# Optimization experiments

Measured on AMD Instinct MI355X. Metric: run time of the kernel, lower is better.

Reference implementation:

```python
import math
import jax, jax.numpy as jnp
import numpy as np

TOPK = 13
NUM_CLASSES = 80
ALPHA = 1.0
BETA = 6.0
EPS = 1e-9


def _ciou(b1, b2, eps=1e-7):
    """CIoU between broadcastable xyxy boxes b1 (gt) and b2 (pred); matches bbox_iou(xywh=False, CIoU=True)."""
    b1x1, b1y1, b1x2, b1y2 = (b1[..., 0], b1[..., 1], b1[..., 2], b1[..., 3])
    b2x1, b2y1, b2x2, b2y2 = (b2[..., 0], b2[..., 1], b2[..., 2], b2[..., 3])
    w1, h1 = b1x2 - b1x1, b1y2 - b1y1 + eps
    w2, h2 = b2x2 - b2x1, b2y2 - b2y1 + eps
    inter = (jnp.clip(jnp.minimum(b1x2, b2x2) - jnp.maximum(b1x1, b2x1), 0.0, None)
             * jnp.clip(jnp.minimum(b1y2, b2y2) - jnp.maximum(b1y1, b2y1), 0.0, None))
    union = w1 * h1 + w2 * h2 - inter + eps
    iou = inter / union
    cw = jnp.maximum(b1x2, b2x2) - jnp.minimum(b1x1, b2x1)
    ch = jnp.maximum(b1y2, b2y2) - jnp.minimum(b1y1, b2y1)
    c2 = cw * cw + ch * ch + eps
    rho2 = ((b2x1 + b2x2 - b1x1 - b1x2) ** 2 + (b2y1 + b2y2 - b1y1 - b1y2) ** 2) / 4.0
    v = (4.0 / math.pi ** 2) * (jnp.arctan(w2 / h2) - jnp.arctan(w1 / h1)) ** 2
    alpha = jax.lax.stop_gradient(v / (v - iou + (1.0 + eps)))  # torch.no_grad() block
    return iou - (rho2 / c2 + v * alpha)


def setup_inputs() -> dict:
    key = jax.random.key(0)
    ks = jax.random.split(key, 7)
    bs, M, nc, img = 16, 128, NUM_CLASSES, 640
    # YOLO anchor points for 640x640, strides 8/16/32 -> 8400 points (pixel coords)
    pts = []
    for s in (8, 16, 32):
        n = img // s
        g = (jnp.arange(n, dtype=jnp.float32) + 0.5) * s
        yv, xv = jnp.meshgrid(g, g, indexing='ij')
        pts.append(jnp.stack([xv, yv], -1).reshape(-1, 2))
    anc_points = jnp.concatenate(pts, 0)  # (8400, 2)
    na = anc_points.shape[0]
    pd_scores = jax.random.uniform(ks[0], (bs, na, nc), dtype=jnp.float32)
    # predicted boxes: xyxy around each anchor point
    cxy = anc_points[None] + jax.random.normal(ks[1], (bs, na, 2)) * 4.0
    wh = jax.random.uniform(ks[2], (bs, na, 2), minval=4.0, maxval=96.0)
    pd_bboxes = jnp.concatenate([cxy - wh / 2, cxy + wh / 2], -1)
    # gt boxes: xyxy in image coords
    g_cxy = jax.random.uniform(ks[3], (bs, M, 2), minval=0.0, maxval=640.0)
    g_wh = jax.random.uniform(ks[4], (bs, M, 2), minval=16.0, maxval=200.0)
    gt_bboxes = jnp.concatenate([g_cxy - g_wh / 2, g_cxy + g_wh / 2], -1)
    gt_labels = jax.random.randint(ks[5], (bs, M, 1), 0, nc, dtype=jnp.int32)
    mask_gt = (jax.random.uniform(ks[6], (bs, M, 1)) < 0.8).astype(jnp.float32)
    return {'pd_scores': pd_scores, 'pd_bboxes': pd_bboxes, 'anc_points': anc_points,
            'gt_labels': gt_labels, 'gt_bboxes': gt_bboxes, 'mask_gt': mask_gt}


def reference(pd_scores, pd_bboxes, anc_points, gt_labels, gt_bboxes, mask_gt):
    bs, na, nc = pd_scores.shape
    M = gt_bboxes.shape[1]
    dt = pd_scores.dtype

    # ---- select_candidates_in_gts: anchor center strictly inside gt box ----
    lt = gt_bboxes[:, :, None, :2]   # (bs,M,1,2)
    rb = gt_bboxes[:, :, None, 2:]   # (bs,M,1,2)
    anc = anc_points[None, None]     # (1,1,na,2)
    d_min = jnp.minimum((anc - lt).min(-1), (rb - anc).min(-1))  # (bs,M,na)
    mask_in_gts = (d_min > EPS).astype(dt)

    # ---- get_box_metrics (dense, masked where torch left zeros) ----
    mask = (mask_in_gts * mask_gt) > 0  # (bs,M,na) bool
    lbl = gt_labels[..., 0]             # (bs,M) int
    # pd_scores[b, :, label] -> (bs,M,na)
    gathered = pd_scores[jnp.arange(bs)[:, None], :, lbl]
    bbox_scores = jnp.where(mask, gathered, 0.0)
    ciou = _ciou(gt_bboxes[:, :, None, :], pd_bboxes[:, None, :, :])  # (bs,M,na)
    overlaps = jnp.where(mask, jnp.clip(ciou, 0.0, None), 0.0)
    align_metric = bbox_scores ** ALPHA * overlaps ** BETA

    # ---- select_topk_candidates ----
    _, topk_idxs = jax.lax.top_k(align_metric, TOPK)            # (bs,M,TOPK)
    topk_idxs = jnp.where(mask_gt > 0, topk_idxs, 0)            # masked_fill_(~topk_mask, 0)
    row_off = (jnp.arange(bs * M, dtype=topk_idxs.dtype) * na).reshape(bs, M, 1)
    counts = (jnp.zeros(bs * M * na, jnp.int32)
              .at[(topk_idxs + row_off).ravel()].add(1)
              .reshape(bs, M, na))
    mask_topk = jnp.where(counts > 1, 0, counts).astype(dt)     # drop anchors hit >1 time per gt

    mask_pos = mask_topk * mask_in_gts * mask_gt                # (bs,M,na)

    # ---- select_highest_overlaps: resolve anchors claimed by multiple gts ----
    fg_mask = mask_pos.sum(1)                                   # (bs,na)
    mask_multi = fg_mask[:, None, :] > 1                        # (bs,1,na)
    max_ov_idx = overlaps.argmax(1)                             # (bs,na)
    is_max = jax.nn.one_hot(max_ov_idx, M, dtype=dt).transpose(0, 2, 1)  # (bs,M,na)
    mask_pos = jnp.where(mask_multi, is_max, mask_pos)
    fg_mask = mask_pos.sum(1)
    target_gt_idx = mask_pos.argmax(1)                          # (bs,na)

    # ---- get_targets ----
    flat_idx = target_gt_idx + jnp.arange(bs, dtype=target_gt_idx.dtype)[:, None] * M
    target_labels = jnp.clip(gt_labels.reshape(-1)[flat_idx], 0, None)     # (bs,na)
    target_bboxes = gt_bboxes.reshape(-1, 4)[flat_idx]                     # (bs,na,4)
    target_scores = jax.nn.one_hot(target_labels, nc, dtype=dt)
    target_scores = jnp.where(fg_mask[..., None] > 0, target_scores, 0.0)

    # ---- normalization of target scores ----
    am = align_metric * mask_pos
    pos_am = am.max(-1, keepdims=True)                          # (bs,M,1)
    pos_ov = (overlaps * mask_pos).max(-1, keepdims=True)       # (bs,M,1)
    norm = (am * pos_ov / (pos_am + EPS)).max(1)[..., None]     # (bs,na,1)
    target_scores = target_scores * norm

    return (target_labels, target_bboxes, target_scores, fg_mask > 0, target_gt_idx)
```

## Files before the change

### kernel.cpp

```cpp
#include <hip/hip_runtime.h>
#include <math.h>

constexpr int BS = 16;
constexpr int NA = 8400;
constexpr int NC = 80;
constexpr int MG = 128;
constexpr int TK = 13;
constexpr int NCAND = 1536;
constexpr int QCAP = 65536;

constexpr int OFF_LBL = 0;
constexpr int OFF_BB  = OFF_LBL + BS * NA;
constexpr int OFF_SC  = OFF_BB  + BS * NA * 4;
constexpr int OFF_FG  = OFF_SC  + BS * NA * NC;
constexpr int OFF_TG  = OFF_FG  + BS * NA;

__device__ __forceinline__ float ciou_pre(float gx, float gy, float gz, float gw,
                                          float px, float py, float pz, float pw,
                                          float dat) {
    const float eps = 1e-7f;
    float w1 = gz - gx, h1 = gw - gy + eps;
    float w2 = pz - px, h2 = pw - py + eps;
    float iw = fmaxf(fminf(gz, pz) - fmaxf(gx, px), 0.f);
    float ih = fmaxf(fminf(gw, pw) - fmaxf(gy, py), 0.f);
    float inter = iw * ih;
    float uni = w1 * h1 + w2 * h2 - inter + eps;
    float iou = inter / uni;
    float cw = fmaxf(gz, pz) - fminf(gx, px);
    float ch = fmaxf(gw, pw) - fminf(gy, py);
    float c2 = cw * cw + ch * ch + eps;
    float dx = px + pz - gx - gz;
    float dy = py + pw - gy - gw;
    float rho2 = (dx * dx + dy * dy) * 0.25f;
    float v = 0.4052847345693511f * dat * dat;
    float alpha = v / (v - iou + (1.f + eps));
    return iou - (rho2 / c2 + v * alpha);
}

__device__ __forceinline__ float ciou_f(float gx, float gy, float gz, float gw,
                                        float px, float py, float pz, float pw) {
    const float eps = 1e-7f;
    float dat = atanf((pz - px) / (pw - py + eps)) - atanf((gz - gx) / (gw - gy + eps));
    return ciou_pre(gx, gy, gz, gw, px, py, pz, pw, dat);
}

__device__ __forceinline__ bool inside_gt(float ax, float ay,
                                          float gx, float gy, float gz, float gw) {
    float d = fminf(fminf(ax - gx, ay - gy), fminf(gz - ax, gw - ay));
    return d > 1e-9f;
}

__device__ __forceinline__ void anchor_xy(int a, float& ax, float& ay) {
    if (a < 6400)      { int iy = a / 80;        int ix = a - iy * 80 - 0;    ax = (ix + 0.5f) * 8.f;  ay = (iy + 0.5f) * 8.f; }
    else if (a < 8000) { int r = a - 6400; int iy = r / 40; int ix = r - iy * 40; ax = (ix + 0.5f) * 16.f; ay = (iy + 0.5f) * 16.f; }
    else               { int r = a - 8000; int iy = r / 20; int ix = r - iy * 20; ax = (ix + 0.5f) * 32.f; ay = (iy + 0.5f) * 32.f; }
}

__global__ __launch_bounds__(64) void k_topk(
    const float* __restrict__ pd_scores, const float* __restrict__ pd_bboxes,
    const int* __restrict__ gt_labels, const float* __restrict__ gt_bboxes,
    const float* __restrict__ mask_gt,
    int* __restrict__ fg_cnt, int* __restrict__ fg_m)
{
    __shared__ float cv[NCAND];
    __shared__ int   ca[NCAND];
    __shared__ int   s_cnt;
    __shared__ unsigned s_pm;

    int bm = blockIdx.x;
    if (mask_gt[bm] <= 0.f) return;
    int b = bm >> 7;
    int m = bm & (MG - 1);
    int tid = threadIdx.x;

    if (tid == 0) { s_cnt = 0; s_pm = 0u; }
    __syncthreads();

    const float4 g = *reinterpret_cast<const float4*>(gt_bboxes + bm * 4);
    const int lbl = gt_labels[bm];
    const float* pbb = pd_bboxes + (size_t)b * NA * 4;
    const float* psc = pd_scores + (size_t)b * NA * NC;
    const float at_g = atanf((g.z - g.x) / (g.w - g.y + 1e-7f));

    auto do_level = [&](float s, int n, int base) {
        int xlo = max(0, (int)floorf(g.x / s - 0.5f) - 1);
        int xhi = min(n - 1, (int)ceilf(g.z / s - 0.5f) + 1);
        int ylo = max(0, (int)floorf(g.y / s - 0.5f) - 1);
        int yhi = min(n - 1, (int)ceilf(g.w / s - 0.5f) + 1);
        int w = xhi - xlo + 1, h = yhi - ylo + 1;
        if (w <= 0 || h <= 0) return;
        int cnt = w * h;
        for (int idx = tid; idx < cnt; idx += 64) {
            int iy = ylo + idx / w;
            int ix = xlo + idx - (idx / w) * w;
            float ax = (ix + 0.5f) * s;
            float ay = (iy + 0.5f) * s;
            if (!inside_gt(ax, ay, g.x, g.y, g.z, g.w)) continue;
            int a = base + iy * n + ix;
            float4 p = *reinterpret_cast<const float4*>(pbb + (size_t)a * 4);
            float dat = atanf((p.z - p.x) / (p.w - p.y + 1e-7f)) - at_g;
            float ov = fmaxf(ciou_pre(g.x, g.y, g.z, g.w, p.x, p.y, p.z, p.w, dat), 0.f);
            float sc = psc[(size_t)a * NC + lbl];
            float ov2 = ov * ov;
            float al = sc * ov2 * ov2 * ov2;
            if (al > 0.f) {
                int slot = atomicAdd(&s_cnt, 1);
                if (slot < NCAND) { cv[slot] = al; ca[slot] = a; }
                if (a < 32) atomicOr(&s_pm, 1u << a);
            }
        }
    };
    do_level(8.f, 80, 0);
    do_level(16.f, 40, 6400);
    do_level(32.f, 20, 8000);
    __syncthreads();

    int npos = min(s_cnt, NCAND);
    int rounds = min(npos, TK);
    int* fgc = fg_cnt + b * NA;
    int* fgm = fg_m + b * NA;

    for (int k = 0; k < rounds; ++k) {
        float bv = -1.f; int bk = 0x7fffffff;
        for (int p = tid; p < npos; p += 64) {
            float v = cv[p];
            int key = (ca[p] << 11) | p;
            if (v > bv || (v == bv && key < bk)) { bv = v; bk = key; }
        }
        #pragma unroll
        for (int off = 32; off > 0; off >>= 1) {
            float v2 = __shfl_down(bv, off);
            int   k2 = __shfl_down(bk, off);
            if (v2 > bv || (v2 == bv && k2 < bk)) { bv = v2; bk = k2; }
        }
        if (tid == 0) {
            int slot = bk & 2047;
            int a = bk >> 11;
            cv[slot] = -1.f;
            atomicAdd(&fgc[a], 1);
            fgm[a] = m;
        }
        __syncthreads();
    }

    if (tid == 0) {
        int need = TK - rounds;
        unsigned pm = s_pm;
        for (int idx = 0; idx < 32 && need > 0; ++idx) {
            if (!((pm >> idx) & 1u)) {
                float ax = (idx + 0.5f) * 8.f, ay = 4.f;
                if (inside_gt(ax, ay, g.x, g.y, g.z, g.w)) {
                    atomicAdd(&fgc[idx], 1);
                    fgm[idx] = m;
                }
                --need;
            }
        }
    }
}

__global__ __launch_bounds__(256) void k_assign(
    const float* __restrict__ pd_scores, const float* __restrict__ pd_bboxes,
    const int* __restrict__ gt_labels, const float* __restrict__ gt_bboxes,
    const float* __restrict__ mask_gt,
    const int* __restrict__ fg_cnt, const int* __restrict__ fg_m,
    float* __restrict__ out, float* __restrict__ am_ws,
    int* __restrict__ gi_ws, int* __restrict__ lbl_ws,
    unsigned* __restrict__ pos_am, unsigned* __restrict__ pos_ov,
    int* __restrict__ multi_cnt, int* __restrict__ multi_q)
{
    __shared__ int s_cnt, s_base;
    int tid = threadIdx.x;
    if (tid == 0) s_cnt = 0;
    __syncthreads();

    int i = blockIdx.x * 256 + tid;
    int cnt = fg_cnt[i];
    bool multi = cnt > 1;

    unsigned long long mk = __ballot(multi);
    int lane = tid & 63;
    int rank = __popcll(mk & ((1ull << lane) - 1ull));
    int wsum = __popcll(mk);
    int wbase = 0;
    if (lane == 0 && wsum) wbase = atomicAdd(&s_cnt, wsum);
    wbase = __shfl(wbase, 0);
    __syncthreads();
    if (tid == 0 && s_cnt) s_base = atomicAdd(multi_cnt, s_cnt);
    __syncthreads();

    if (multi) {
        multi_q[s_base + wbase + rank] = i;
        return;
    }

    int b = i / NA, a = i - b * NA;
    int t = (cnt == 1) ? fg_m[i] : 0;
    int gi = b * MG + t;
    float4 g = *reinterpret_cast<const float4*>(gt_bboxes + gi * 4);
    int lraw = gt_labels[gi];
    int lbl = max(lraw, 0);

    if (cnt == 1) {
        float am = 0.f, ovv = 0.f;
        if (mask_gt[gi] > 0.f) {
            float ax, ay; anchor_xy(a, ax, ay);
            if (inside_gt(ax, ay, g.x, g.y, g.z, g.w)) {
                float4 p = *reinterpret_cast<const float4*>(pd_bboxes + (size_t)i * 4);
                float ov = fmaxf(ciou_f(g.x, g.y, g.z, g.w, p.x, p.y, p.z, p.w), 0.f);
                float sc = pd_scores[(size_t)i * NC + lraw];
                float ov2 = ov * ov;
                am = sc * ov2 * ov2 * ov2;
                ovv = ov;
            }
        }
        atomicMax(&pos_am[gi], __float_as_uint(am));
        atomicMax(&pos_ov[gi], __float_as_uint(ovv));
        am_ws[i] = am; gi_ws[i] = gi; lbl_ws[i] = lbl;
    } else {
        gi_ws[i] = -1;
    }

    out[OFF_LBL + i] = (float)lbl;
    reinterpret_cast<float4*>(out + OFF_BB)[i] = g;
    out[OFF_FG + i] = cnt ? 1.f : 0.f;
    out[OFF_TG + i] = (float)t;
}

__global__ __launch_bounds__(256) void k_fix(
    const float* __restrict__ pd_scores, const float* __restrict__ pd_bboxes,
    const int* __restrict__ gt_labels, const float* __restrict__ gt_bboxes,
    const float* __restrict__ mask_gt,
    const int* __restrict__ multi_cnt, const int* __restrict__ multi_q,
    float* __restrict__ out, float* __restrict__ am_ws,
    int* __restrict__ gi_ws, int* __restrict__ lbl_ws,
    unsigned* __restrict__ pos_am, unsigned* __restrict__ pos_ov)
{
    int gtid = blockIdx.x * 256 + threadIdx.x;
    int wave = gtid >> 6;
    int lane = gtid & 63;
    int nwaves = (gridDim.x * 256) >> 6;
    int qn = *multi_cnt;

    for (int qi = wave; qi < qn; qi += nwaves) {
        int i = multi_q[qi];
        int b = i / NA, a = i - b * NA;
        float ax, ay; anchor_xy(a, ax, ay);
        float4 p = *reinterpret_cast<const float4*>(pd_bboxes + (size_t)i * 4);
        float at_p = atanf((p.z - p.x) / (p.w - p.y + 1e-7f));

        auto ovm = [&](int mm) -> float {
            int gi = b * MG + mm;
            float ov = 0.f;
            if (mask_gt[gi] > 0.f) {
                float4 gg = *reinterpret_cast<const float4*>(gt_bboxes + gi * 4);
                if (inside_gt(ax, ay, gg.x, gg.y, gg.z, gg.w)) {
                    float dat = at_p - atanf((gg.z - gg.x) / (gg.w - gg.y + 1e-7f));
                    ov = fmaxf(ciou_pre(gg.x, gg.y, gg.z, gg.w, p.x, p.y, p.z, p.w, dat), 0.f);
                }
            }
            return ov;
        };
        float ov0 = ovm(lane);
        float ov1 = ovm(lane + 64);
        float bov; int bm_;
        if (ov1 > ov0) { bov = ov1; bm_ = lane + 64; }
        else           { bov = ov0; bm_ = lane; }
        #pragma unroll
        for (int off = 32; off > 0; off >>= 1) {
            float v2 = __shfl_down(bov, off);
            int   m2 = __shfl_down(bm_, off);
            if (v2 > bov || (v2 == bov && m2 < bm_)) { bov = v2; bm_ = m2; }
        }
        if (lane == 0) {
            int t = bm_;
            int gi = b * MG + t;
            int lraw = gt_labels[gi];
            int lbl = max(lraw, 0);
            float am = 0.f;
            if (bov > 0.f) {
                float sc = pd_scores[(size_t)i * NC + lraw];
                float o2 = bov * bov;
                am = sc * o2 * o2 * o2;
            }
            atomicMax(&pos_am[gi], __float_as_uint(am));
            atomicMax(&pos_ov[gi], __float_as_uint(bov));
            float4 g = *reinterpret_cast<const float4*>(gt_bboxes + gi * 4);
            out[OFF_LBL + i] = (float)lbl;
            reinterpret_cast<float4*>(out + OFF_BB)[i] = g;
            out[OFF_FG + i] = 1.f;
            out[OFF_TG + i] = (float)t;
            am_ws[i] = am; gi_ws[i] = gi; lbl_ws[i] = lbl;
        }
    }
}

__global__ __launch_bounds__(256) void k_scatter(
    const float* __restrict__ am_ws, const int* __restrict__ gi_ws,
    const int* __restrict__ lbl_ws,
    const unsigned* __restrict__ pos_am, const unsigned* __restrict__ pos_ov,
    float* __restrict__ out_scores)
{
    int i = blockIdx.x * 256 + threadIdx.x;
    if (i >= BS * NA) return;
    int gi = gi_ws[i];
    if (gi >= 0) {
        float norm = am_ws[i] * __uint_as_float(pos_ov[gi]) /
                     (__uint_as_float(pos_am[gi]) + 1e-9f);
        out_scores[(size_t)i * NC + lbl_ws[i]] = norm;
    }
}

extern "C" void kernel_launch(void* const* d_in, const int* in_sizes, int n_in,
                              void* d_out, int out_size, void* d_ws, size_t ws_size,
                              hipStream_t stream) {
    const float* pd_scores = (const float*)d_in[0];
    const float* pd_bboxes = (const float*)d_in[1];
    const int*   gt_labels = (const int*)d_in[3];
    const float* gt_bboxes = (const float*)d_in[4];
    const float* mask_gt   = (const float*)d_in[5];
    float* out = (float*)d_out;

    unsigned char* w = (unsigned char*)d_ws;
    size_t off = 0;
    int*      fg_cnt    = (int*)(w + off);      off += (size_t)BS * NA * 4;
    unsigned* pos_am    = (unsigned*)(w + off); off += (size_t)BS * MG * 4;
    unsigned* pos_ov    = (unsigned*)(w + off); off += (size_t)BS * MG * 4;
    int*      multi_cnt = (int*)(w + off);      off += 4;
    size_t zero_bytes = off;
    int*      fg_m      = (int*)(w + off);      off += (size_t)BS * NA * 4;
    float*    am_ws     = (float*)(w + off);    off += (size_t)BS * NA * 4;
    int*      gi_ws     = (int*)(w + off);      off += (size_t)BS * NA * 4;
    int*      lbl_ws    = (int*)(w + off);      off += (size_t)BS * NA * 4;
    int*      multi_q   = (int*)(w + off);      off += (size_t)QCAP * 4;

    hipMemsetAsync(w, 0, zero_bytes, stream);
    hipMemsetAsync(out + OFF_SC, 0, (size_t)BS * NA * NC * sizeof(float), stream);

    k_topk<<<BS * MG, 64, 0, stream>>>(pd_scores, pd_bboxes, gt_labels,
                                       gt_bboxes, mask_gt, fg_cnt, fg_m);

    int nA = BS * NA;
    k_assign<<<nA / 256, 256, 0, stream>>>(
        pd_scores, pd_bboxes, gt_labels, gt_bboxes, mask_gt,
        fg_cnt, fg_m, out, am_ws, gi_ws, lbl_ws, pos_am, pos_ov,
        multi_cnt, multi_q);

    k_fix<<<2048, 256, 0, stream>>>(
        pd_scores, pd_bboxes, gt_labels, gt_bboxes, mask_gt,
        multi_cnt, multi_q, out, am_ws, gi_ws, lbl_ws, pos_am, pos_ov);

    k_scatter<<<nA / 256, 256, 0, stream>>>(am_ws, gi_ws, lbl_ws,
                                            pos_am, pos_ov, out + OFF_SC);
}
```

Measured before the change: 152.8 us.

## Fold multi-assignment fix into assign kernel and write dense scores without memset

Removes the separate k_fix kernel and its work queue: anchors claimed by several GTs now loop over all 128 GTs inside k_assign, reusing GT arctan values cached per GT by k_topk. The large memset of the score tensor plus the sparse scatter is replaced by one kernel that writes every score row as float4, zero or normalized. k_topk moves to 128-thread blocks with a two-wave reduction. This cuts launches and one full pass over the score buffer. The cost is that multi-assigned anchors are resolved serially per thread inside divergent wavefronts.

```diff
diff --git a/kernel.cpp b/kernel.cpp
--- a/kernel.cpp
+++ b/kernel.cpp
@@ -7,7 +7,6 @@
 constexpr int MG = 128;
 constexpr int TK = 13;
 constexpr int NCAND = 1536;
-constexpr int QCAP = 65536;
 
 constexpr int OFF_LBL = 0;
 constexpr int OFF_BB  = OFF_LBL + BS * NA;
@@ -37,13 +36,6 @@
     return iou - (rho2 / c2 + v * alpha);
 }
 
-__device__ __forceinline__ float ciou_f(float gx, float gy, float gz, float gw,
-                                        float px, float py, float pz, float pw) {
-    const float eps = 1e-7f;
-    float dat = atanf((pz - px) / (pw - py + eps)) - atanf((gz - gx) / (gw - gy + eps));
-    return ciou_pre(gx, gy, gz, gw, px, py, pz, pw, dat);
-}
-
 __device__ __forceinline__ bool inside_gt(float ax, float ay,
                                           float gx, float gy, float gz, float gw) {
     float d = fminf(fminf(ax - gx, ay - gy), fminf(gz - ax, gw - ay));
@@ -51,21 +43,24 @@
 }
 
 __device__ __forceinline__ void anchor_xy(int a, float& ax, float& ay) {
-    if (a < 6400)      { int iy = a / 80;        int ix = a - iy * 80 - 0;    ax = (ix + 0.5f) * 8.f;  ay = (iy + 0.5f) * 8.f; }
+    if (a < 6400)      { int iy = a / 80;        int ix = a - iy * 80;           ax = (ix + 0.5f) * 8.f;  ay = (iy + 0.5f) * 8.f; }
     else if (a < 8000) { int r = a - 6400; int iy = r / 40; int ix = r - iy * 40; ax = (ix + 0.5f) * 16.f; ay = (iy + 0.5f) * 16.f; }
     else               { int r = a - 8000; int iy = r / 20; int ix = r - iy * 20; ax = (ix + 0.5f) * 32.f; ay = (iy + 0.5f) * 32.f; }
 }
 
-__global__ __launch_bounds__(64) void k_topk(
+__global__ __launch_bounds__(128) void k_topk(
     const float* __restrict__ pd_scores, const float* __restrict__ pd_bboxes,
     const int* __restrict__ gt_labels, const float* __restrict__ gt_bboxes,
     const float* __restrict__ mask_gt,
-    int* __restrict__ fg_cnt, int* __restrict__ fg_m)
+    int* __restrict__ fg_cnt, int* __restrict__ fg_m,
+    float* __restrict__ at_g_tbl)
 {
     __shared__ float cv[NCAND];
     __shared__ int   ca[NCAND];
     __shared__ int   s_cnt;
     __shared__ unsigned s_pm;
+    __shared__ float s_wv[2];
+    __shared__ int   s_wk[2];
 
     int bm = blockIdx.x;
     if (mask_gt[bm] <= 0.f) return;
@@ -81,6 +76,7 @@
     const float* pbb = pd_bboxes + (size_t)b * NA * 4;
     const float* psc = pd_scores + (size_t)b * NA * NC;
     const float at_g = atanf((g.z - g.x) / (g.w - g.y + 1e-7f));
+    if (tid == 0) at_g_tbl[bm] = at_g;
 
     auto do_level = [&](float s, int n, int base) {
         int xlo = max(0, (int)floorf(g.x / s - 0.5f) - 1);
@@ -90,7 +86,7 @@
         int w = xhi - xlo + 1, h = yhi - ylo + 1;
         if (w <= 0 || h <= 0) return;
         int cnt = w * h;
-        for (int idx = tid; idx < cnt; idx += 64) {
+        for (int idx = tid; idx < cnt; idx += 128) {
             int iy = ylo + idx / w;
             int ix = xlo + idx - (idx / w) * w;
             float ax = (ix + 0.5f) * s;
@@ -122,7 +118,7 @@
 
     for (int k = 0; k < rounds; ++k) {
         float bv = -1.f; int bk = 0x7fffffff;
-        for (int p = tid; p < npos; p += 64) {
+        for (int p = tid; p < npos; p += 128) {
             float v = cv[p];
             int key = (ca[p] << 11) | p;
             if (v > bv || (v == bv && key < bk)) { bv = v; bk = key; }
@@ -133,7 +129,11 @@
             int   k2 = __shfl_down(bk, off);
             if (v2 > bv || (v2 == bv && k2 < bk)) { bv = v2; bk = k2; }
         }
+        int wid = tid >> 6;
+        if ((tid & 63) == 0) { s_wv[wid] = bv; s_wk[wid] = bk; }
+        __syncthreads();
         if (tid == 0) {
+            if (s_wv[1] > bv || (s_wv[1] == bv && s_wk[1] < bk)) { bv = s_wv[1]; bk = s_wk[1]; }
             int slot = bk & 2047;
             int a = bk >> 11;
             cv[slot] = -1.f;
@@ -162,58 +162,69 @@
 __global__ __launch_bounds__(256) void k_assign(
     const float* __restrict__ pd_scores, const float* __restrict__ pd_bboxes,
     const int* __restrict__ gt_labels, const float* __restrict__ gt_bboxes,
-    const float* __restrict__ mask_gt,
+    const float* __restrict__ mask_gt, const float* __restrict__ at_g_tbl,
     const int* __restrict__ fg_cnt, const int* __restrict__ fg_m,
     float* __restrict__ out, float* __restrict__ am_ws,
     int* __restrict__ gi_ws, int* __restrict__ lbl_ws,
-    unsigned* __restrict__ pos_am, unsigned* __restrict__ pos_ov,
-    int* __restrict__ multi_cnt, int* __restrict__ multi_q)
+    unsigned* __restrict__ pos_am, unsigned* __restrict__ pos_ov)
 {
-    __shared__ int s_cnt, s_base;
-    int tid = threadIdx.x;
-    if (tid == 0) s_cnt = 0;
-    __syncthreads();
-
-    int i = blockIdx.x * 256 + tid;
+    int i = blockIdx.x * 256 + threadIdx.x;
     int cnt = fg_cnt[i];
+    int b = i / NA, a = i - b * NA;
+    int gbase = b * MG;
+
+    int t = 0;
+    float bov = -1.f;
     bool multi = cnt > 1;
-
-    unsigned long long mk = __ballot(multi);
-    int lane = tid & 63;
-    int rank = __popcll(mk & ((1ull << lane) - 1ull));
-    int wsum = __popcll(mk);
-    int wbase = 0;
-    if (lane == 0 && wsum) wbase = atomicAdd(&s_cnt, wsum);
-    wbase = __shfl(wbase, 0);
-    __syncthreads();
-    if (tid == 0 && s_cnt) s_base = atomicAdd(multi_cnt, s_cnt);
-    __syncthreads();
-
     if (multi) {
-        multi_q[s_base + wbase + rank] = i;
-        return;
-    }
-
-    int b = i / NA, a = i - b * NA;
-    int t = (cnt == 1) ? fg_m[i] : 0;
-    int gi = b * MG + t;
+        float ax, ay; anchor_xy(a, ax, ay);
+        float4 p = *reinterpret_cast<const float4*>(pd_bboxes + (size_t)i * 4);
+        float at_p = atanf((p.z - p.x) / (p.w - p.y + 1e-7f));
+        for (int mm = 0; mm < MG; ++mm) {
+            int gi = gbase + mm;
+            float ov = 0.f;
+            if (mask_gt[gi] > 0.f) {
+                float4 gg = *reinterpret_cast<const float4*>(gt_bboxes + gi * 4);
+                if (inside_gt(ax, ay, gg.x, gg.y, gg.z, gg.w)) {
+                    float dat = at_p - at_g_tbl[gi];
+                    ov = fmaxf(ciou_pre(gg.x, gg.y, gg.z, gg.w, p.x, p.y, p.z, p.w, dat), 0.f);
+                }
+            }
+            if (ov > bov) { bov = ov; t = mm; }
+        }
+    } else if (cnt == 1) {
+        t = fg_m[i];
+    }
+
+    int gi = gbase + t;
     float4 g = *reinterpret_cast<const float4*>(gt_bboxes + gi * 4);
     int lraw = gt_labels[gi];
     int lbl = max(lraw, 0);
 
-    if (cnt == 1) {
-        float am = 0.f, ovv = 0.f;
+    float am = 0.f, ovv = 0.f;
+    if (multi) {
+        if (bov > 0.f) {
+            float sc = pd_scores[(size_t)i * NC + lraw];
+            float o2 = bov * bov;
+            am = sc * o2 * o2 * o2;
+            ovv = bov;
+        }
+    } else if (cnt == 1) {
         if (mask_gt[gi] > 0.f) {
             float ax, ay; anchor_xy(a, ax, ay);
             if (inside_gt(ax, ay, g.x, g.y, g.z, g.w)) {
                 float4 p = *reinterpret_cast<const float4*>(pd_bboxes + (size_t)i * 4);
-                float ov = fmaxf(ciou_f(g.x, g.y, g.z, g.w, p.x, p.y, p.z, p.w), 0.f);
+                float dat = atanf((p.z - p.x) / (p.w - p.y + 1e-7f)) - at_g_tbl[gi];
+                float ov = fmaxf(ciou_pre(g.x, g.y, g.z, g.w, p.x, p.y, p.z, p.w, dat), 0.f);
                 float sc = pd_scores[(size_t)i * NC + lraw];
                 float ov2 = ov * ov;
                 am = sc * ov2 * ov2 * ov2;
                 ovv = ov;
             }
         }
+    }
+
+    if (cnt > 0) {
         atomicMax(&pos_am[gi], __float_as_uint(am));
         atomicMax(&pos_ov[gi], __float_as_uint(ovv));
         am_ws[i] = am; gi_ws[i] = gi; lbl_ws[i] = lbl;
@@ -227,88 +238,27 @@
     out[OFF_TG + i] = (float)t;
 }
 
-__global__ __launch_bounds__(256) void k_fix(
-    const float* __restrict__ pd_scores, const float* __restrict__ pd_bboxes,
-    const int* __restrict__ gt_labels, const float* __restrict__ gt_bboxes,
-    const float* __restrict__ mask_gt,
-    const int* __restrict__ multi_cnt, const int* __restrict__ multi_q,
-    float* __restrict__ out, float* __restrict__ am_ws,
-    int* __restrict__ gi_ws, int* __restrict__ lbl_ws,
-    unsigned* __restrict__ pos_am, unsigned* __restrict__ pos_ov)
-{
-    int gtid = blockIdx.x * 256 + threadIdx.x;
-    int wave = gtid >> 6;
-    int lane = gtid & 63;
-    int nwaves = (gridDim.x * 256) >> 6;
-    int qn = *multi_cnt;
-
-    for (int qi = wave; qi < qn; qi += nwaves) {
-        int i = multi_q[qi];
-        int b = i / NA, a = i - b * NA;
-        float ax, ay; anchor_xy(a, ax, ay);
-        float4 p = *reinterpret_cast<const float4*>(pd_bboxes + (size_t)i * 4);
-        float at_p = atanf((p.z - p.x) / (p.w - p.y + 1e-7f));
-
-        auto ovm = [&](int mm) -> float {
-            int gi = b * MG + mm;
-            float ov = 0.f;
-            if (mask_gt[gi] > 0.f) {
-                float4 gg = *reinterpret_cast<const float4*>(gt_bboxes + gi * 4);
-                if (inside_gt(ax, ay, gg.x, gg.y, gg.z, gg.w)) {
-                    float dat = at_p - atanf((gg.z - gg.x) / (gg.w - gg.y + 1e-7f));
-                    ov = fmaxf(ciou_pre(gg.x, gg.y, gg.z, gg.w, p.x, p.y, p.z, p.w, dat), 0.f);
-                }
-            }
-            return ov;
-        };
-        float ov0 = ovm(lane);
-        float ov1 = ovm(lane + 64);
-        float bov; int bm_;
-        if (ov1 > ov0) { bov = ov1; bm_ = lane + 64; }
-        else           { bov = ov0; bm_ = lane; }
-        #pragma unroll
-        for (int off = 32; off > 0; off >>= 1) {
-            float v2 = __shfl_down(bov, off);
-            int   m2 = __shfl_down(bm_, off);
-            if (v2 > bov || (v2 == bov && m2 < bm_)) { bov = v2; bm_ = m2; }
-        }
-        if (lane == 0) {
-            int t = bm_;
-            int gi = b * MG + t;
-            int lraw = gt_labels[gi];
-            int lbl = max(lraw, 0);
-            float am = 0.f;
-            if (bov > 0.f) {
-                float sc = pd_scores[(size_t)i * NC + lraw];
-                float o2 = bov * bov;
-                am = sc * o2 * o2 * o2;
-            }
-            atomicMax(&pos_am[gi], __float_as_uint(am));
-            atomicMax(&pos_ov[gi], __float_as_uint(bov));
-            float4 g = *reinterpret_cast<const float4*>(gt_bboxes + gi * 4);
-            out[OFF_LBL + i] = (float)lbl;
-            reinterpret_cast<float4*>(out + OFF_BB)[i] = g;
-            out[OFF_FG + i] = 1.f;
-            out[OFF_TG + i] = (float)t;
-            am_ws[i] = am; gi_ws[i] = gi; lbl_ws[i] = lbl;
-        }
-    }
-}
-
-__global__ __launch_bounds__(256) void k_scatter(
+__global__ __launch_bounds__(256) void k_scores(
     const float* __restrict__ am_ws, const int* __restrict__ gi_ws,
     const int* __restrict__ lbl_ws,
     const unsigned* __restrict__ pos_am, const unsigned* __restrict__ pos_ov,
     float* __restrict__ out_scores)
 {
-    int i = blockIdx.x * 256 + threadIdx.x;
-    if (i >= BS * NA) return;
+    constexpr int NQ = NC / 4;
+    int idx = blockIdx.x * 256 + threadIdx.x;
+    int i = idx / NQ;
+    int q = idx - i * NQ;
+    float4 v = {0.f, 0.f, 0.f, 0.f};
     int gi = gi_ws[i];
     if (gi >= 0) {
-        float norm = am_ws[i] * __uint_as_float(pos_ov[gi]) /
-                     (__uint_as_float(pos_am[gi]) + 1e-9f);
-        out_scores[(size_t)i * NC + lbl_ws[i]] = norm;
-    }
+        int lbl = lbl_ws[i];
+        if ((lbl >> 2) == q) {
+            float norm = am_ws[i] * __uint_as_float(pos_ov[gi]) /
+                         (__uint_as_float(pos_am[gi]) + 1e-9f);
+            reinterpret_cast<float*>(&v)[lbl & 3] = norm;
+        }
+    }
+    reinterpret_cast<float4*>(out_scores)[idx] = v;
 }
 
 extern "C" void kernel_launch(void* const* d_in, const int* in_sizes, int n_in,
@@ -323,33 +273,27 @@
 
     unsigned char* w = (unsigned char*)d_ws;
     size_t off = 0;
-    int*      fg_cnt    = (int*)(w + off);      off += (size_t)BS * NA * 4;
-    unsigned* pos_am    = (unsigned*)(w + off); off += (size_t)BS * MG * 4;
-    unsigned* pos_ov    = (unsigned*)(w + off); off += (size_t)BS * MG * 4;
-    int*      multi_cnt = (int*)(w + off);      off += 4;
+    int*      fg_cnt   = (int*)(w + off);      off += (size_t)BS * NA * 4;
+    unsigned* pos_am   = (unsigned*)(w + off); off += (size_t)BS * MG * 4;
+    unsigned* pos_ov   = (unsigned*)(w + off); off += (size_t)BS * MG * 4;
     size_t zero_bytes = off;
-    int*      fg_m      = (int*)(w + off);      off += (size_t)BS * NA * 4;
-    float*    am_ws     = (float*)(w + off);    off += (size_t)BS * NA * 4;
-    int*      gi_ws     = (int*)(w + off);      off += (size_t)BS * NA * 4;
-    int*      lbl_ws    = (int*)(w + off);      off += (size_t)BS * NA * 4;
-    int*      multi_q   = (int*)(w + off);      off += (size_t)QCAP * 4;
+    int*      fg_m     = (int*)(w + off);      off += (size_t)BS * NA * 4;
+    float*    am_ws    = (float*)(w + off);    off += (size_t)BS * NA * 4;
+    int*      gi_ws    = (int*)(w + off);      off += (size_t)BS * NA * 4;
+    int*      lbl_ws   = (int*)(w + off);      off += (size_t)BS * NA * 4;
+    float*    at_g_tbl = (float*)(w + off);    off += (size_t)BS * MG * 4;
 
     hipMemsetAsync(w, 0, zero_bytes, stream);
-    hipMemsetAsync(out + OFF_SC, 0, (size_t)BS * NA * NC * sizeof(float), stream);
-
-    k_topk<<<BS * MG, 64, 0, stream>>>(pd_scores, pd_bboxes, gt_labels,
-                                       gt_bboxes, mask_gt, fg_cnt, fg_m);
+
+    k_topk<<<BS * MG, 128, 0, stream>>>(pd_scores, pd_bboxes, gt_labels,
+                                        gt_bboxes, mask_gt, fg_cnt, fg_m,
+                                        at_g_tbl);
 
     int nA = BS * NA;
     k_assign<<<nA / 256, 256, 0, stream>>>(
-        pd_scores, pd_bboxes, gt_labels, gt_bboxes, mask_gt,
-        fg_cnt, fg_m, out, am_ws, gi_ws, lbl_ws, pos_am, pos_ov,
-        multi_cnt, multi_q);
-
-    k_fix<<<2048, 256, 0, stream>>>(
-        pd_scores, pd_bboxes, gt_labels, gt_bboxes, mask_gt,
-        multi_cnt, multi_q, out, am_ws, gi_ws, lbl_ws, pos_am, pos_ov);
-
-    k_scatter<<<nA / 256, 256, 0, stream>>>(am_ws, gi_ws, lbl_ws,
-                                            pos_am, pos_ov, out + OFF_SC);
-}
+        pd_scores, pd_bboxes, gt_labels, gt_bboxes, mask_gt, at_g_tbl,
+        fg_cnt, fg_m, out, am_ws, gi_ws, lbl_ws, pos_am, pos_ov);
+
+    k_scores<<<nA * (NC / 4) / 256, 256, 0, stream>>>(
+        am_ws, gi_ws, lbl_ws, pos_am, pos_ov, out + OFF_SC);
+}
```

Result: slower. 183.4 us (+20.0%).
